# Performance work log

Hardware: AMD Instinct MI355X
Metric: run time of the kernel (lower is better)

Reference implementation:

```python
import jax, jax.numpy as jnp
import numpy as np
from jax import lax


def ternary_quant(w):
    # Layer-wise ternary quantization: alpha = mean(|w|), threshold = 0.001*alpha
    alpha = lax.stop_gradient(jnp.mean(jnp.abs(w)))
    thr = 0.001 * alpha
    q = jnp.where(w > thr, 1.0, jnp.where(w < -thr, -1.0, 0.0))
    return alpha * q


def setup_inputs() -> dict:
    key = jax.random.key(0)
    k1, k2, k3, k4, k5 = jax.random.split(key, 5)
    B, C, H, W = 32, 384, 64, 64
    fan_in = C * 3 * 3
    bound = 1.0 / np.sqrt(fan_in)  # torch Conv2d default init scale
    return {
        "x": jax.random.normal(k1, (B, C, H, W), dtype=jnp.float32),
        "weight": jax.random.uniform(k2, (C, C, 3, 3), dtype=jnp.float32, minval=-bound, maxval=bound),
        "bias": jax.random.uniform(k3, (C,), dtype=jnp.float32, minval=-bound, maxval=bound),
        "time_emb": jax.random.normal(k4, (B, 512), dtype=jnp.float32),
        "y": jax.random.randint(k5, (B,), 0, 1000, dtype=jnp.int64),
    }


def reference(x, weight, bias, time_emb, y):
    # time_emb and y are accepted but unused, matching Downsample.forward
    qw = ternary_quant(weight)
    out = lax.conv_general_dilated(
        x, qw,
        window_strides=(2, 2),
        padding=((1, 1), (1, 1)),
        dimension_numbers=("NCHW", "OIHW", "NCHW"),
    )
    return out + bias[None, :, None, None]
```

## Files before the change

kernel.cpp:

```cpp
#include <hip/hip_runtime.h>
#include <hip/hip_bf16.h>


#define CIN   384
#define HIN   64
#define WIN   64
#define OHW   32
#define KDIM  3456
#define NWELT 1327104
#define MDIM  32768
#define NT    54

using bf16 = __hip_bfloat16;
typedef __attribute__((ext_vector_type(8))) short short8;
typedef __attribute__((ext_vector_type(4))) float floatx4;
typedef __attribute__((ext_vector_type(2))) unsigned short ushort2v;

#define AS1 __attribute__((address_space(1)))
#define AS3 __attribute__((address_space(3)))
#define DMA16(g, l) __builtin_amdgcn_global_load_lds((const AS1 void*)(g), (AS3 void*)(l), 16, 0, 0)

#define EDGE_V(N) do { \
    asm volatile("s_waitcnt vmcnt(" #N ")" ::: "memory"); \
    __builtin_amdgcn_s_barrier(); \
    __builtin_amdgcn_sched_barrier(0); \
} while (0)

#define NPART  62
#define ZG_F   16
#define XN_OFF 256
#define WQ_OFF (256 + 100663296)

__global__ void absum_part(const float* __restrict__ w, float* __restrict__ ws) {
    const float4* w4 = (const float4*)w;
    float s = 0.f;
    for (int i = blockIdx.x * 256 + threadIdx.x; i < NWELT / 4; i += NPART * 256) {
        float4 v = w4[i];
        s += fabsf(v.x) + fabsf(v.y) + fabsf(v.z) + fabsf(v.w);
    }
    for (int off = 32; off; off >>= 1) s += __shfl_down(s, off, 64);
    __shared__ float red[4];
    if ((threadIdx.x & 63) == 0) red[threadIdx.x >> 6] = s;
    __syncthreads();
    if (threadIdx.x == 0) ws[2 + blockIdx.x] = red[0] + red[1] + red[2] + red[3];
}

__global__ void absum_final(float* __restrict__ ws) {
    if (threadIdx.x == 0) {
        float s = 0.f;
        for (int i = 0; i < NPART; ++i) s += ws[2 + i];
        float alpha = s * (1.0f / NWELT);
        ws[0] = alpha;
        ws[1] = 1e-3f * alpha;
        ws[ZG_F + 0] = 0.f; ws[ZG_F + 1] = 0.f;
        ws[ZG_F + 2] = 0.f; ws[ZG_F + 3] = 0.f;
    }
}

__global__ void quant_kernel(const float* __restrict__ w, const float* __restrict__ ws,
                             bf16* __restrict__ wq) {
    int j = blockIdx.x * 256 + threadIdx.x;
    if (j >= NWELT) return;
    float thr = ws[1];
    int o = j / KDIM;
    int rmd = j - o * KDIM;
    int khkw = rmd / 384;
    int c = rmd - khkw * 384;
    float v = w[((o * 384 + c) * 9) + khkw];
    float q = (v > thr) ? 1.f : ((v < -thr) ? -1.f : 0.f);
    wq[j] = __float2bfloat16(q);
}

__global__ void nhwc_kernel(const float* __restrict__ x, bf16* __restrict__ xn) {
    int nh = blockIdx.x;
    int n = nh >> 6, h = nh & 63;
    int c0 = blockIdx.y * 64;
    __shared__ bf16 tile[64][66];
    const float* src = x + ((n * CIN + c0) * HIN + h) * WIN;
    for (int i = 0; i < 4; ++i) {
        int s = threadIdx.x + i * 256;
        int cl = s >> 4, w4 = (s & 15) * 4;
        float4 v = *(const float4*)(src + cl * 4096 + w4);
        bf16 t0[2], t1[2];
        t0[0] = __float2bfloat16(v.x); t0[1] = __float2bfloat16(v.y);
        t1[0] = __float2bfloat16(v.z); t1[1] = __float2bfloat16(v.w);
        *(ushort2v*)&tile[cl][w4]     = *(ushort2v*)t0;
        *(ushort2v*)&tile[cl][w4 + 2] = *(ushort2v*)t1;
    }
    __syncthreads();
    bf16* dst = xn + ((size_t)(n * HIN + h) * WIN) * CIN + c0;
    for (int i = 0; i < 2; ++i) {
        int q = threadIdx.x + i * 256;
        int wc = q >> 3, c8 = (q & 7) * 8;
        bf16 tmp[8];
        #pragma unroll
        for (int j = 0; j < 8; ++j) tmp[j] = tile[c8 + j][wc];
        *(short8*)(dst + (size_t)wc * CIN + c8) = *(short8*)tmp;
    }
}

#define BM  128
#define BN  128

__global__ __launch_bounds__(256, 2) void conv_gemm(const bf16* __restrict__ xn,
                                                    const bf16* __restrict__ wq,
                                                    const float* __restrict__ ws,
                                                    const float* __restrict__ bias,
                                                    float* __restrict__ out,
                                                    const bf16* __restrict__ zg) {
    __shared__ __align__(16) bf16 lW[2][BN * 64];
    __shared__ __align__(16) bf16 lX[3][BM * 64];
    const int m_base = blockIdx.x * BM;
    const int o_base = blockIdx.y * BN;
    const int tid = threadIdx.x;
    const int lane = tid & 63;
    const int wv = tid >> 6;
    const int wo = (wv & 1) * 64;
    const int wm = (wv >> 1) * 64;
    const int g = (lane & 7) ^ (lane >> 3);

    const bf16* pw[4];
    const bf16* pxn[4];
    int oh2[4], ow2[4], wLoff[4], xLoff[4];
    #pragma unroll
    for (int i = 0; i < 4; ++i) {
        int rr = (wv * 4 + i) * 8;
        wLoff[i] = rr * 64;
        xLoff[i] = rr * 64;
        pw[i] = wq + (size_t)(o_base + rr + (lane >> 3)) * KDIM + g * 8;
        int m = m_base + rr + (lane >> 3);
        int n = m >> 10, oh = (m >> 5) & 31, ow = m & 31;
        pxn[i] = xn + (size_t)n * (HIN * WIN * CIN) + g * 8;
        oh2[i] = 2 * oh - 1;
        ow2[i] = 2 * ow - 1;
    }

    const int l15 = lane & 15, quad = lane >> 4, l7 = lane & 7;

    floatx4 acc[4][4];
    #pragma unroll
    for (int i = 0; i < 4; ++i)
        #pragma unroll
        for (int j = 0; j < 4; ++j)
            acc[i][j] = (floatx4){0.f, 0.f, 0.f, 0.f};

    {
        #pragma unroll
        for (int i = 0; i < 4; ++i) {
            int ih = oh2[i], iw = ow2[i];
            const bf16* p = (ih >= 0 && iw >= 0) ? pxn[i] + (ih * WIN + iw) * CIN : zg;
            DMA16(p, &lX[0][xLoff[i]]);
        }
        #pragma unroll
        for (int i = 0; i < 4; ++i)
            DMA16(pw[i], &lW[0][wLoff[i]]);
        #pragma unroll
        for (int i = 0; i < 4; ++i) {
            int ih = oh2[i], iw = ow2[i];
            const bf16* p = (ih >= 0 && iw >= 0) ? pxn[i] + (ih * WIN + iw) * CIN + 64 : zg;
            DMA16(p, &lX[1][xLoff[i]]);
        }
        EDGE_V(4);
    }

    for (int t = 0; t < NT - 1; ++t) {
        const bf16* lWc = lW[t & 1];
        const bf16* lXc = lX[t % 3];
        bf16* lWn = lW[(t + 1) & 1];
        bf16* lXn2 = lX[(t + 2) % 3];
        const int kW = (t + 1) * 64;
        const int s2 = t + 2;
        const int khkw2 = s2 / 6, cc2 = s2 - khkw2 * 6;
        const int kh2 = khkw2 / 3, kw2 = khkw2 - kh2 * 3;

        short8 af[2][4], bfr[2][4];
        #pragma unroll
        for (int ks = 0; ks < 2; ++ks) {
            const int oct = ((ks * 4 + quad) ^ l7) * 8;
            #pragma unroll
            for (int i = 0; i < 4; ++i)
                af[ks][i] = *(const short8*)(lWc + (wo + i * 16 + l15) * 64 + oct);
            #pragma unroll
            for (int j = 0; j < 4; ++j)
                bfr[ks][j] = *(const short8*)(lXc + (wm + j * 16 + l15) * 64 + oct);
        }

        #pragma unroll
        for (int i = 0; i < 4; ++i)
            DMA16(pw[i] + kW, lWn + wLoff[i]);
        #pragma unroll
        for (int i = 0; i < 4; ++i) {
            int ih = oh2[i] + kh2, iw = ow2[i] + kw2;
            bool valid = (ih >= 0) & (iw >= 0) & (s2 < NT);
            const bf16* p = valid ? pxn[i] + (ih * WIN + iw) * CIN + cc2 * 64 : zg;
            DMA16(p, lXn2 + xLoff[i]);
        }

        __builtin_amdgcn_s_setprio(1);
        #pragma unroll
        for (int ks = 0; ks < 2; ++ks)
            #pragma unroll
            for (int i = 0; i < 4; ++i)
                #pragma unroll
                for (int j = 0; j < 4; ++j)
                    acc[i][j] = __builtin_amdgcn_mfma_f32_16x16x32_bf16(
                        af[ks][i], bfr[ks][j], acc[i][j], 0, 0, 0);
        __builtin_amdgcn_s_setprio(0);

        EDGE_V(4);
    }

    {
        const bf16* lWc = lW[1];
        const bf16* lXc = lX[53 % 3];
        short8 af[2][4], bfr[2][4];
        #pragma unroll
        for (int ks = 0; ks < 2; ++ks) {
            const int oct = ((ks * 4 + quad) ^ l7) * 8;
            #pragma unroll
            for (int i = 0; i < 4; ++i)
                af[ks][i] = *(const short8*)(lWc + (wo + i * 16 + l15) * 64 + oct);
            #pragma unroll
            for (int j = 0; j < 4; ++j)
                bfr[ks][j] = *(const short8*)(lXc + (wm + j * 16 + l15) * 64 + oct);
        }
        __builtin_amdgcn_s_setprio(1);
        #pragma unroll
        for (int ks = 0; ks < 2; ++ks)
            #pragma unroll
            for (int i = 0; i < 4; ++i)
                #pragma unroll
                for (int j = 0; j < 4; ++j)
                    acc[i][j] = __builtin_amdgcn_mfma_f32_16x16x32_bf16(
                        af[ks][i], bfr[ks][j], acc[i][j], 0, 0, 0);
        __builtin_amdgcn_s_setprio(0);
    }

    float alpha = ws[0];
    #pragma unroll
    for (int i = 0; i < 4; ++i) {
        #pragma unroll
        for (int j = 0; j < 4; ++j) {
            int mm = m_base + wm + j * 16 + l15;
            int n = mm >> 10, oh = (mm >> 5) & 31, ow = mm & 31;
            #pragma unroll
            for (int r = 0; r < 4; ++r) {
                int o = o_base + wo + i * 16 + quad * 4 + r;
                out[((n * 384 + o) * OHW + oh) * OHW + ow] = alpha * acc[i][j][r] + bias[o];
            }
        }
    }
}

extern "C" void kernel_launch(void* const* d_in, const int* in_sizes, int n_in,
                              void* d_out, int out_size, void* d_ws, size_t ws_size,
                              hipStream_t stream) {
    (void)in_sizes; (void)n_in; (void)out_size; (void)ws_size;
    const float* x    = (const float*)d_in[0];
    const float* w    = (const float*)d_in[1];
    const float* bias = (const float*)d_in[2];
    float* out = (float*)d_out;
    float* wsf = (float*)d_ws;
    bf16* xn = (bf16*)((char*)d_ws + XN_OFF);
    bf16* wq = (bf16*)((char*)d_ws + WQ_OFF);
    const bf16* zg = (const bf16*)(wsf + ZG_F);

    absum_part<<<NPART, 256, 0, stream>>>(w, wsf);
    absum_final<<<1, 64, 0, stream>>>(wsf);
    quant_kernel<<<(NWELT + 255) / 256, 256, 0, stream>>>(w, wsf, wq);
    nhwc_kernel<<<dim3(2048, 6), 256, 0, stream>>>(x, xn);
    conv_gemm<<<dim3(MDIM / BM, 384 / BN), 256, 0, stream>>>(xn, wq, wsf, bias, out, zg);
}
```

Baseline: 444.5 us.

## Shrink LDS buffering to raise occupancy to three blocks per CU

Cuts LDS staging from two weight plus three activation buffers to a single weight buffer and two activation buffers, and raises launch bounds from 2 to 3 blocks per CU. The prefetch depth drops from two stages to one. The weight tile is refilled in place after an extra barrier that waits for the LDS fragment reads, and each step ends with a full vmcnt(0) wait. The aim is more resident waves to hide latency, at the cost of less in-flight prefetch, an extra barrier per K step, and register pressure under the tighter launch bound.

```diff
diff --git a/kernel.cpp b/kernel.cpp
--- a/kernel.cpp
+++ b/kernel.cpp
@@ -20,8 +20,13 @@
 #define AS3 __attribute__((address_space(3)))
 #define DMA16(g, l) __builtin_amdgcn_global_load_lds((const AS1 void*)(g), (AS3 void*)(l), 16, 0, 0)
 
-#define EDGE_V(N) do { \
-    asm volatile("s_waitcnt vmcnt(" #N ")" ::: "memory"); \
+#define EDGE_L() do { \
+    asm volatile("s_waitcnt lgkmcnt(0)" ::: "memory"); \
+    __builtin_amdgcn_s_barrier(); \
+    __builtin_amdgcn_sched_barrier(0); \
+} while (0)
+#define EDGE_V0() do { \
+    asm volatile("s_waitcnt vmcnt(0)" ::: "memory"); \
     __builtin_amdgcn_s_barrier(); \
     __builtin_amdgcn_sched_barrier(0); \
 } while (0)
@@ -102,14 +107,14 @@
 #define BM  128
 #define BN  128
 
-__global__ __launch_bounds__(256, 2) void conv_gemm(const bf16* __restrict__ xn,
+__global__ __launch_bounds__(256, 3) void conv_gemm(const bf16* __restrict__ xn,
                                                     const bf16* __restrict__ wq,
                                                     const float* __restrict__ ws,
                                                     const float* __restrict__ bias,
                                                     float* __restrict__ out,
                                                     const bf16* __restrict__ zg) {
-    __shared__ __align__(16) bf16 lW[2][BN * 64];
-    __shared__ __align__(16) bf16 lX[3][BM * 64];
+    __shared__ __align__(16) bf16 lW[BN * 64];
+    __shared__ __align__(16) bf16 lX[2][BM * 64];
     const int m_base = blockIdx.x * BM;
     const int o_base = blockIdx.y * BN;
     const int tid = threadIdx.x;
@@ -153,25 +158,25 @@
         }
         #pragma unroll
         for (int i = 0; i < 4; ++i)
-            DMA16(pw[i], &lW[0][wLoff[i]]);
+            DMA16(pw[i], &lW[wLoff[i]]);
+        EDGE_V0();
+    }
+
+    for (int t = 0; t < NT - 1; ++t) {
+        const bf16* lXc = lX[t & 1];
+        bf16* lXn = lX[(t + 1) & 1];
+        const int kW = (t + 1) * 64;
+        const int s1 = t + 1;
+        const int khkw1 = s1 / 6, cc1 = s1 - khkw1 * 6;
+        const int kh1 = khkw1 / 3, kw1 = khkw1 - kh1 * 3;
+
         #pragma unroll
         for (int i = 0; i < 4; ++i) {
-            int ih = oh2[i], iw = ow2[i];
-            const bf16* p = (ih >= 0 && iw >= 0) ? pxn[i] + (ih * WIN + iw) * CIN + 64 : zg;
-            DMA16(p, &lX[1][xLoff[i]]);
-        }
-        EDGE_V(4);
-    }
-
-    for (int t = 0; t < NT - 1; ++t) {
-        const bf16* lWc = lW[t & 1];
-        const bf16* lXc = lX[t % 3];
-        bf16* lWn = lW[(t + 1) & 1];
-        bf16* lXn2 = lX[(t + 2) % 3];
-        const int kW = (t + 1) * 64;
-        const int s2 = t + 2;
-        const int khkw2 = s2 / 6, cc2 = s2 - khkw2 * 6;
-        const int kh2 = khkw2 / 3, kw2 = khkw2 - kh2 * 3;
+            int ih = oh2[i] + kh1, iw = ow2[i] + kw1;
+            bool valid = (ih >= 0) & (iw >= 0);
+            const bf16* p = valid ? pxn[i] + (ih * WIN + iw) * CIN + cc1 * 64 : zg;
+            DMA16(p, lXn + xLoff[i]);
+        }
 
         short8 af[2][4], bfr[2][4];
         #pragma unroll
@@ -179,22 +184,17 @@
             const int oct = ((ks * 4 + quad) ^ l7) * 8;
             #pragma unroll
             for (int i = 0; i < 4; ++i)
-                af[ks][i] = *(const short8*)(lWc + (wo + i * 16 + l15) * 64 + oct);
+                af[ks][i] = *(const short8*)(lW + (wo + i * 16 + l15) * 64 + oct);
             #pragma unroll
             for (int j = 0; j < 4; ++j)
                 bfr[ks][j] = *(const short8*)(lXc + (wm + j * 16 + l15) * 64 + oct);
         }
 
+        EDGE_L();
+
         #pragma unroll
         for (int i = 0; i < 4; ++i)
-            DMA16(pw[i] + kW, lWn + wLoff[i]);
-        #pragma unroll
-        for (int i = 0; i < 4; ++i) {
-            int ih = oh2[i] + kh2, iw = ow2[i] + kw2;
-            bool valid = (ih >= 0) & (iw >= 0) & (s2 < NT);
-            const bf16* p = valid ? pxn[i] + (ih * WIN + iw) * CIN + cc2 * 64 : zg;
-            DMA16(p, lXn2 + xLoff[i]);
-        }
+            DMA16(pw[i] + kW, lW + wLoff[i]);
 
         __builtin_amdgcn_s_setprio(1);
         #pragma unroll
@@ -207,19 +207,18 @@
                         af[ks][i], bfr[ks][j], acc[i][j], 0, 0, 0);
         __builtin_amdgcn_s_setprio(0);
 
-        EDGE_V(4);
+        EDGE_V0();
     }
 
     {
-        const bf16* lWc = lW[1];
-        const bf16* lXc = lX[53 % 3];
+        const bf16* lXc = lX[53 & 1];
         short8 af[2][4], bfr[2][4];
         #pragma unroll
         for (int ks = 0; ks < 2; ++ks) {
             const int oct = ((ks * 4 + quad) ^ l7) * 8;
             #pragma unroll
             for (int i = 0; i < 4; ++i)
-                af[ks][i] = *(const short8*)(lWc + (wo + i * 16 + l15) * 64 + oct);
+                af[ks][i] = *(const short8*)(lW + (wo + i * 16 + l15) * 64 + oct);
             #pragma unroll
             for (int j = 0; j < 4; ++j)
                 bfr[ks][j] = *(const short8*)(lXc + (wm + j * 16 + l15) * 64 + oct);
```

Result: no change. 445.9 us (+0.3%).
